# Kernel tuning notes

Measured on AMD Instinct MI355X. Metric: run time of the kernel, lower is better.

The kernel has to match this reference:

```python
import jax, jax.numpy as jnp
import numpy as np

B, T, C = 2, 2048, 1024
H, D, R = 16, 64, 32  # heads, head_dim, compression rank (R < D)


def setup_inputs() -> dict:
    key = jax.random.key(0)
    ks = jax.random.split(key, 8)
    s = 0.02
    return {
        "hidden_states": jax.random.normal(ks[0], (B, T, C), jnp.float32),
        "c_attn_w": jax.random.normal(ks[1], (C, 3 * C), jnp.float32) * s,
        "c_attn_b": jnp.zeros((3 * C,), jnp.float32),
        "c_proj_w": jax.random.normal(ks[2], (C, C), jnp.float32) * s,
        "c_proj_b": jnp.zeros((C,), jnp.float32),
        "wk_c": jax.random.normal(ks[3], (D, R), jnp.float32) * (1.0 / np.sqrt(D)),
        "wk_e": jax.random.normal(ks[4], (R, D), jnp.float32) * (1.0 / np.sqrt(R)),
        "wv_c": jax.random.normal(ks[5], (D, R), jnp.float32) * (1.0 / np.sqrt(D)),
        "wv_e": jax.random.normal(ks[6], (R, D), jnp.float32) * (1.0 / np.sqrt(R)),
    }


def reference(hidden_states, c_attn_w, c_attn_b, c_proj_w, c_proj_b,
              wk_c, wk_e, wv_c, wv_e):
    b, t, c = hidden_states.shape
    # GPT2 Conv1D: x @ W + b, then split into Q, K, V
    qkv = hidden_states @ c_attn_w + c_attn_b  # [B,T,3C]
    q, k, v = jnp.split(qkv, 3, axis=-1)

    def split_heads(x):  # [B,T,C] -> [B,H,T,D]
        return x.reshape(b, t, H, D).transpose(0, 2, 1, 3)

    q = split_heads(q)
    k = split_heads(k)
    v = split_heads(v)

    # Low-rank KV compression then expansion (rank R < D path)
    k_lat = jnp.einsum('bhtd,dr->bhtr', k, wk_c)  # [B,H,T,R]
    v_lat = jnp.einsum('bhtd,dr->bhtr', v, wv_c)
    k_exp = jnp.einsum('bhtr,rd->bhtd', k_lat, wk_e)  # [B,H,T,D]
    v_exp = jnp.einsum('bhtr,rd->bhtd', v_lat, wv_e)

    # Causal SDPA (attention_mask is None and q_len > 1 -> is_causal=True)
    scale = 1.0 / np.sqrt(D).astype(np.float32)
    scores = jnp.einsum('bhqd,bhkd->bhqk', q, k_exp) * scale  # [B,H,T,T]
    causal = jnp.tril(jnp.ones((t, t), dtype=bool))
    scores = jnp.where(causal[None, None], scores, jnp.finfo(scores.dtype).min)
    probs = jax.nn.softmax(scores, axis=-1)
    attn = jnp.einsum('bhqk,bhkd->bhqd', probs, v_exp)  # [B,H,T,D]

    # Merge heads and output projection
    attn = attn.transpose(0, 2, 1, 3).reshape(b, t, c)
    out = attn @ c_proj_w + c_proj_b
    return out
```

## Files before the change

kernel.cpp:

```cpp
#include <hip/hip_runtime.h>
#include <cstddef>

typedef __attribute__((ext_vector_type(8))) __bf16 bf16x8;
typedef __attribute__((ext_vector_type(4))) float f32x4;
typedef unsigned short u16;
typedef unsigned int   u32;

#define SCLF (0.125f * 1.44269504f)

__device__ __forceinline__ u16 f2bf(float f){
  union { float f; u32 u; } v; v.f = f;
  u32 r = v.u + 0x7FFFu + ((v.u >> 16) & 1u);
  return (u16)(r >> 16);
}
__device__ __forceinline__ u32 cvtpk(float lo, float hi){
  u32 r; asm("v_cvt_pk_bf16_f32 %0, %1, %2" : "=v"(r) : "v"(lo), "v"(hi)); return r;
}
__device__ __forceinline__ void gll16(const void* g, void* l){
  __builtin_amdgcn_global_load_lds((__attribute__((address_space(1))) void*)g,
                                   (__attribute__((address_space(3))) void*)l, 16, 0, 0);
}

__global__ __launch_bounds__(256) void convert_all(const float* __restrict__ x,
      const float* __restrict__ Wa, const float* __restrict__ ba,
      const float* __restrict__ kc, const float* __restrict__ ke,
      const float* __restrict__ vc, const float* __restrict__ ve,
      u16* __restrict__ Xb, u16* __restrict__ Wab, u16* __restrict__ Mb,
      float* __restrict__ b2){
  __shared__ float BaL[1024];
  __shared__ float W65[32*65];
  const int bid = blockIdx.x, tid = threadIdx.x;
  if (bid < 4096){
    int i = bid*256 + tid;
    float4 v = ((const float4*)x)[i];
    ushort4 r; r.x=f2bf(v.x); r.y=f2bf(v.y); r.z=f2bf(v.z); r.w=f2bf(v.w);
    ((ushort4*)Xb)[i] = r;
  } else if (bid < 7168){
    int i = (bid-4096)*256 + tid;
    float4 v = ((const float4*)Wa)[i];
    ushort4 r; r.x=f2bf(v.x); r.y=f2bf(v.y); r.z=f2bf(v.z); r.w=f2bf(v.w);
    ((ushort4*)Wab)[i] = r;
  } else if (bid == 7168){
    #pragma unroll
    for (int t=0;t<8;++t){
      int idx = t*256 + tid;
      Mb[idx] = f2bf(ke[idx]*SCLF);
      int d = idx>>5, r = idx&31;
      Mb[2048 + r*64 + d] = f2bf(kc[idx]);
      Mb[4096 + r*64 + d] = f2bf(vc[idx]);
      Mb[6144 + idx] = f2bf(ve[idx]);
    }
  } else {
    const int part = bid - 7169;
    *(float4*)&BaL[tid*4] = *(const float4*)&ba[part*1024 + tid*4];
    {
      const float* msrc = (part==0) ? ke : (part==1) ? kc : vc;
      #pragma unroll
      for (int i=0;i<8;++i){
        int idx = tid + i*256;
        float v = msrc[idx];
        int r, d;
        if (part == 0){ r = idx >> 6; d = idx & 63; }
        else          { d = idx >> 5; r = idx & 31; }
        W65[r*65 + d] = v;
      }
    }
    __syncthreads();
    const float scl = (part==0) ? SCLF : 1.f;
    #pragma unroll
    for (int t=0;t<2;++t){
      int l = tid + t*256;
      int hh = l >> 5, r = l & 31;
      float acc = 0.f;
      for (int d=0;d<64;++d) acc += BaL[hh*64 + d] * W65[r*65 + d];
      b2[part*512 + l] = acc * scl;
    }
  }
}

__global__ __launch_bounds__(256) void transpose_cvt(const float* __restrict__ src, int ld_src,
            u16* __restrict__ dst, int ld_dst){
  __shared__ float tile[64][65];
  int c0 = blockIdx.x*64, n0 = blockIdx.y*64;
  int tx = threadIdx.x & 63, ty = threadIdx.x >> 6;
  #pragma unroll 4
  for (int k=0;k<16;++k){
    int r = 4*k + ty;
    tile[r][tx] = src[(size_t)(c0+r)*ld_src + n0 + tx];
  }
  __syncthreads();
  #pragma unroll 4
  for (int k=0;k<16;++k){
    int r = 4*k + ty;
    dst[(size_t)(n0+r)*ld_dst + c0 + tx] = f2bf(tile[tx][r]);
  }
}

__global__ __launch_bounds__(256) void fold_gemm_qkv(const u16* __restrict__ Wab,
      const u16* __restrict__ Mb, u16* __restrict__ Wt){
  __shared__ u16 As[4096];
  __shared__ u16 Bs[2048];
  const int cc = blockIdx.x, ph = blockIdx.y;
  const int tid = threadIdx.x, wv = tid>>6, ln = tid&63;
  const int lr = ln&15, g8 = (ln>>4)*8, gq = ln>>4;
  const int c0 = cc*64;
  const u16* A = Wab + (size_t)c0*3072 + ph*64;
  const u16* B = Mb + (ph>>4)*2048;
  const int lrow = ln>>3, lcol = (ln&7)*8;
  #pragma unroll
  for (int it=0;it<3;++it){
    int c3 = wv*3 + it;
    if (c3 < 8) gll16(A + (size_t)(c3*8+lrow)*3072 + lcol, &As[c3*512]);
    else { int bc = c3-8; gll16(B + (bc*8+lrow)*64 + lcol, &Bs[bc*512]); }
  }
  __syncthreads();
  f32x4 acc[2] = {};
  const int wr = (wv>>1)*32, wn = wv&1;
  #pragma unroll
  for (int ks=0;ks<2;++ks){
    bf16x8 bf = *(const bf16x8*)&Bs[(wn*16+lr)*64 + ks*32 + g8];
    #pragma unroll
    for (int mt=0;mt<2;++mt){
      bf16x8 af = *(const bf16x8*)&As[(wr+mt*16+lr)*64 + ks*32 + g8];
      acc[mt] = __builtin_amdgcn_mfma_f32_16x16x32_bf16(af, bf, acc[mt], 0,0,0);
    }
  }
  const int n = (ph>>4)*512 + (ph&15)*32 + wn*16 + lr;
  #pragma unroll
  for (int mt=0;mt<2;++mt){
    union { u16 s[4]; uint2 v; } pk;
    #pragma unroll
    for (int r=0;r<4;++r) pk.s[r] = f2bf(acc[mt][r]);
    *(uint2*)&Wt[(size_t)n*1024 + c0 + wr + mt*16 + 4*gq] = pk.v;
  }
}

__global__ __launch_bounds__(256) void fold_gemm_proj(const u16* __restrict__ WpTb,
      const u16* __restrict__ veb, u16* __restrict__ W2t){
  __shared__ u16 As[4096];
  __shared__ u16 Bs[2048];
  const int cc = blockIdx.x, ph = blockIdx.y;
  const int tid = threadIdx.x, wv = tid>>6, ln = tid&63;
  const int lr = ln&15, g8 = (ln>>4)*8, gq = ln>>4;
  const int c0 = cc*64;
  const u16* A = WpTb + (size_t)c0*1024 + ph*64;
  const int lrow = ln>>3, lcol = (ln&7)*8;
  #pragma unroll
  for (int it=0;it<3;++it){
    int c3 = wv*3 + it;
    if (c3 < 8) gll16(A + (size_t)(c3*8+lrow)*1024 + lcol, &As[c3*512]);
    else { int bc = c3-8; gll16(veb + (bc*8+lrow)*64 + lcol, &Bs[bc*512]); }
  }
  __syncthreads();
  f32x4 acc[2] = {};
  const int wr = (wv>>1)*32, wn = wv&1;
  #pragma unroll
  for (int ks=0;ks<2;++ks){
    bf16x8 bf = *(const bf16x8*)&Bs[(wn*16+lr)*64 + ks*32 + g8];
    #pragma unroll
    for (int mt=0;mt<2;++mt){
      bf16x8 af = *(const bf16x8*)&As[(wr+mt*16+lr)*64 + ks*32 + g8];
      acc[mt] = __builtin_amdgcn_mfma_f32_16x16x32_bf16(af, bf, acc[mt], 0,0,0);
    }
  }
  const int col = ph*32 + wn*16 + lr;
  #pragma unroll
  for (int mt=0;mt<2;++mt)
    #pragma unroll
    for (int r=0;r<4;++r)
      W2t[(size_t)(c0 + wr + mt*16 + 4*gq + r)*512 + col] = f2bf(acc[mt][r]);
}

template<typename OT>
__global__ __launch_bounds__(256) void gemm64(const u16* __restrict__ A, const u16* __restrict__ Bt,
        const float* __restrict__ bias, OT* __restrict__ C, u16* __restrict__ Vt,
        int M, int N, int K, int ldc){
  __shared__ u16 As[64*64];
  __shared__ u16 Bs[128*64];
  const int nwg = gridDim.x * gridDim.y;
  const int id  = blockIdx.x + gridDim.x * blockIdx.y;
  const int nid = (id & 7) * (nwg >> 3) + (id >> 3);
  const int bx = nid % gridDim.x, by = nid / gridDim.x;
  const int tid = threadIdx.x, wv = tid>>6, ln = tid&63;
  const int lr = ln&15, g8 = (ln>>4)*8;
  const int m0 = bx*64, n0 = by*128;
  const int wr = (wv>>1)*32, wc = (wv&1)*64;
  const int lrow = ln>>3, lcol = (ln&7)*8;
  f32x4 acc[2][4] = {};
  const int nk = K >> 6;
  for (int kt=0; kt<nk; ++kt){
    #pragma unroll
    for (int it=0; it<6; ++it){
      int chunk = wv*6 + it;
      if (chunk < 8){
        int row = chunk*8 + lrow;
        gll16(A + (size_t)(m0+row)*K + kt*64 + lcol, &As[chunk*512]);
      } else {
        int bc = chunk - 8;
        int row = bc*8 + lrow;
        gll16(Bt + (size_t)(n0+row)*K + kt*64 + lcol, &Bs[bc*512]);
      }
    }
    __syncthreads();
    #pragma unroll
    for (int ks=0; ks<2; ++ks){
      bf16x8 af[2], bfr[4];
      #pragma unroll
      for (int mt=0;mt<2;++mt) af[mt]  = *(const bf16x8*)&As[(wr+mt*16+lr)*64 + ks*32 + g8];
      #pragma unroll
      for (int nt=0;nt<4;++nt) bfr[nt] = *(const bf16x8*)&Bs[(wc+nt*16+lr)*64 + ks*32 + g8];
      #pragma unroll
      for (int mt=0;mt<2;++mt)
        #pragma unroll
        for (int nt=0;nt<4;++nt)
          acc[mt][nt] = __builtin_amdgcn_mfma_f32_16x16x32_bf16(af[mt], bfr[nt], acc[mt][nt], 0,0,0);
    }
    __syncthreads();
  }
  if (Vt && n0 >= 1024){
    #pragma unroll
    for (int mt=0;mt<2;++mt){
      int row0 = m0 + wr + mt*16 + 4*(ln>>4);
      int tin  = row0 & 2047;
      int p0 = 4*((tin>>4)&1) + 8*((tin>>2)&3) + 32*(tin>>5);
      size_t vbase = (size_t)(row0 >> 11) * 512;
      #pragma unroll
      for (int nt=0;nt<4;++nt){
        int col = n0 + wc + nt*16 + lr;
        float bv = bias[col];
        int nlat = col - 1024;
        union { u16 s[4]; uint2 v; } pk;
        #pragma unroll
        for (int r=0;r<4;++r) pk.s[r] = f2bf(acc[mt][nt][r] + bv);
        *(uint2*)&Vt[(vbase + nlat)*2048 + p0] = pk.v;
      }
    }
  } else {
    #pragma unroll
    for (int mt=0;mt<2;++mt){
      int row = m0 + wr + mt*16 + 4*(ln>>4);
      #pragma unroll
      for (int nt=0;nt<4;++nt){
        int col = n0 + wc + nt*16 + lr;
        float bv = bias[col];
        #pragma unroll
        for (int r=0;r<4;++r){
          float v = acc[mt][nt][r] + bv;
          if constexpr (sizeof(OT) == 2) C[(size_t)(row+r)*ldc + col] = f2bf(v);
          else                           C[(size_t)(row+r)*ldc + col] = v;
        }
      }
    }
  }
}

__global__ __launch_bounds__(512, 8) void attn_fwd(const u16* __restrict__ QKV,
            const u16* __restrict__ Vt, u16* __restrict__ Out){
  const int bh = blockIdx.x;
  const int qt = 31 - blockIdx.y;
  const int b = bh >> 4, h = bh & 15;
  const int tid = threadIdx.x, wv = tid>>6, ln = tid&63;
  const int sg = wv>>2, wvL = wv&3;
  const int lr = ln&15, gq = ln>>4;
  __shared__ __align__(16) char SMEM[32768];
  u16* KB0 = (u16*)SMEM           + (sg*2    )*2048;
  u16* KB1 = (u16*)SMEM           + (sg*2 + 1)*2048;
  u16* VB0 = (u16*)(SMEM + 16384) + (sg*2    )*2048;
  u16* VB1 = (u16*)(SMEM + 16384) + (sg*2 + 1)*2048;
  const int q0 = qt*64;
  const size_t base = (size_t)(b*2048) * 1536;
  bf16x8 qf = *(const bf16x8*)(QKV + base + (size_t)(q0 + wvL*16 + lr)*1536 + h*32 + gq*8);
  const int qglob = q0 + wvL*16 + lr;
  f32x4 o0 = {}, o1 = {};
  float l_r = 0.f;
  const u16* ksrc = QKV + base + 512 + h*32;
  const u16* vsrc = Vt + (size_t)(bh*32)*2048;

  const int ci = wvL*64 + ln;
  const int rK = ci>>2, cK = 8*((ci&3) ^ (rK&3));
  const int rV = ci>>3, cV = 8*((ci&7) ^ (rV&7));

  int offK[4], offV[2][2];
  #pragma unroll
  for (int nt=0;nt<4;++nt)
    offK[nt] = (nt*16+lr)*64 + ((gq*16) ^ ((lr&3)<<4));
  #pragma unroll
  for (int dt=0;dt<2;++dt)
    #pragma unroll
    for (int c=0;c<2;++c)
      offV[dt][c] = (dt*16+lr)*128 + ((c*64 + gq*16) ^ ((lr&7)<<4));

  if (sg <= qt){
    gll16(ksrc + (size_t)(sg*64 + rK)*1536 + cK, KB0 + wvL*512);
    gll16(vsrc + (size_t)rV*2048 + sg*64 + cV,   VB0 + wvL*512);
  }
  __syncthreads();
  const u16* kp = ksrc + (size_t)(sg*64 + 128 + rK)*1536 + cK;
  const u16* vp = vsrc + (size_t)rV*2048 + sg*64 + 128 + cV;
  const size_t KSTEP = (size_t)128*1536;

  #define ABODY(II, KBC, VBC, KBN, VBN) do { \
    const int kt = 2*(II) + sg; \
    if (kt + 2 <= qt){ \
      gll16(kp, (KBN) + wvL*512); \
      gll16(vp, (VBN) + wvL*512); \
      kp += KSTEP; vp += 128; \
    } \
    if (kt <= qt){ \
      f32x4 s4[4] = {}; \
      __builtin_amdgcn_s_setprio(1); \
      _Pragma("unroll") for (int nt=0;nt<4;++nt){ \
        bf16x8 k0 = *(const bf16x8*)((const char*)(KBC) + offK[nt]); \
        s4[nt] = __builtin_amdgcn_mfma_f32_16x16x32_bf16(k0, qf, s4[nt], 0,0,0); \
      } \
      __builtin_amdgcn_s_setprio(0); \
      if (kt == qt){ \
        const int kv0 = kt*64; \
        _Pragma("unroll") for (int nt=0;nt<4;++nt) \
        _Pragma("unroll") for (int r=0;r<4;++r){ \
          int k = kv0 + nt*16 + 4*gq + r; \
          if (k > qglob) s4[nt][r] = -1e30f; \
        } \
      } \
      float p0,p1,p2,p3,p4,p5,p6,p7; \
      p0=__builtin_amdgcn_exp2f(s4[0][0]); p1=__builtin_amdgcn_exp2f(s4[0][1]); \
      p2=__builtin_amdgcn_exp2f(s4[0][2]); p3=__builtin_amdgcn_exp2f(s4[0][3]); \
      p4=__builtin_amdgcn_exp2f(s4[1][0]); p5=__builtin_amdgcn_exp2f(s4[1][1]); \
      p6=__builtin_amdgcn_exp2f(s4[1][2]); p7=__builtin_amdgcn_exp2f(s4[1][3]); \
      l_r += ((p0+p1)+(p2+p3)) + ((p4+p5)+(p6+p7)); \
      union { u32 u[4]; bf16x8 v; } pa0, pa1; \
      pa0.u[0]=cvtpk(p0,p1); pa0.u[1]=cvtpk(p2,p3); pa0.u[2]=cvtpk(p4,p5); pa0.u[3]=cvtpk(p6,p7); \
      p0=__builtin_amdgcn_exp2f(s4[2][0]); p1=__builtin_amdgcn_exp2f(s4[2][1]); \
      p2=__builtin_amdgcn_exp2f(s4[2][2]); p3=__builtin_amdgcn_exp2f(s4[2][3]); \
      p4=__builtin_amdgcn_exp2f(s4[3][0]); p5=__builtin_amdgcn_exp2f(s4[3][1]); \
      p6=__builtin_amdgcn_exp2f(s4[3][2]); p7=__builtin_amdgcn_exp2f(s4[3][3]); \
      l_r += ((p0+p1)+(p2+p3)) + ((p4+p5)+(p6+p7)); \
      pa1.u[0]=cvtpk(p0,p1); pa1.u[1]=cvtpk(p2,p3); pa1.u[2]=cvtpk(p4,p5); pa1.u[3]=cvtpk(p6,p7); \
      __builtin_amdgcn_s_setprio(1); \
      o0 = __builtin_amdgcn_mfma_f32_16x16x32_bf16(pa0.v, *(const bf16x8*)((const char*)(VBC) + offV[0][0]), o0, 0,0,0); \
      o1 = __builtin_amdgcn_mfma_f32_16x16x32_bf16(pa0.v, *(const bf16x8*)((const char*)(VBC) + offV[1][0]), o1, 0,0,0); \
      o0 = __builtin_amdgcn_mfma_f32_16x16x32_bf16(pa1.v, *(const bf16x8*)((const char*)(VBC) + offV[0][1]), o0, 0,0,0); \
      o1 = __builtin_amdgcn_mfma_f32_16x16x32_bf16(pa1.v, *(const bf16x8*)((const char*)(VBC) + offV[1][1]), o1, 0,0,0); \
      __builtin_amdgcn_s_setprio(0); \
    } \
    __syncthreads(); \
  } while(0)

  const int nmax = (qt + 2) >> 1;
  const int jmax = (nmax + 1) >> 1;
  for (int j = 0; j < jmax; ++j){
    ABODY(2*j,   KB0, VB0, KB1, VB1);
    ABODY(2*j+1, KB1, VB1, KB0, VB0);
  }
  l_r += __shfl_xor(l_r, 16);
  l_r += __shfl_xor(l_r, 32);

  float* MO = (float*)SMEM;
  float* ML = (float*)(SMEM + 12288);
  if (sg == 1){
    #pragma unroll
    for (int r=0;r<4;++r){
      MO[(wvL*16 + 4*gq + r)*34 + lr]      = o0[r];
      MO[(wvL*16 + 4*gq + r)*34 + 16 + lr] = o1[r];
    }
    if (gq == 0) ML[wvL*16 + lr] = l_r;
  }
  __syncthreads();
  if (sg == 0){
    float lS = l_r + ML[wvL*16 + lr];
    float lS_o[4];
    #pragma unroll
    for (int r=0;r<4;++r) lS_o[r] = __shfl(lS, 4*gq + r);
    #pragma unroll
    for (int r=0;r<4;++r){
      int orow = wvL*16 + 4*gq + r;
      float v0 = (o0[r] + MO[orow*34 + lr])      / lS_o[r];
      float v1 = (o1[r] + MO[orow*34 + 16 + lr]) / lS_o[r];
      size_t ob = (size_t)(b*2048 + q0 + orow)*512 + h*32;
      Out[ob + lr]      = f2bf(v0);
      Out[ob + 16 + lr] = f2bf(v1);
    }
  }
}

#define WS_B2   0u
#define WS_WT   8192u
#define WS_W2T  (WS_WT + 3145728u)
#define WS_XB   (WS_W2T + 1048576u)
#define WS_QKV  (WS_XB + 8388608u)
#define WS_VT   (WS_QKV + 12582912u)
#define WS_ATT  (WS_VT + 4194304u)
#define WS_WAB  (WS_ATT + 4194304u)
#define WS_WPT  (WS_WAB + 6291456u)
#define WS_MB   (WS_WPT + 2097152u)

extern "C" void kernel_launch(void* const* d_in, const int* in_sizes, int n_in,
                              void* d_out, int out_size, void* d_ws, size_t ws_size,
                              hipStream_t stream) {
  const float* x  = (const float*)d_in[0];
  const float* Wa = (const float*)d_in[1];
  const float* ba = (const float*)d_in[2];
  const float* Wp = (const float*)d_in[3];
  const float* bp = (const float*)d_in[4];
  const float* kc = (const float*)d_in[5];
  const float* ke = (const float*)d_in[6];
  const float* vc = (const float*)d_in[7];
  const float* ve = (const float*)d_in[8];
  float* out = (float*)d_out;
  char* ws = (char*)d_ws;
  float* b2  = (float*)(ws + WS_B2);
  u16* Wt    = (u16*)(ws + WS_WT);
  u16* W2t   = (u16*)(ws + WS_W2T);
  u16* Xb    = (u16*)(ws + WS_XB);
  u16* QKVb  = (u16*)(ws + WS_QKV);
  u16* Vt    = (u16*)(ws + WS_VT);
  u16* Att   = (u16*)(ws + WS_ATT);
  u16* Wab   = (u16*)(ws + WS_WAB);
  u16* WpTb  = (u16*)(ws + WS_WPT);
  u16* Mb    = (u16*)(ws + WS_MB);
  u16* veb   = Mb + 6144;

  convert_all<<<7172, 256, 0, stream>>>(x, Wa, ba, kc, ke, vc, ve, Xb, Wab, Mb, b2);
  transpose_cvt<<<dim3(16,16), 256, 0, stream>>>(Wp, 1024, WpTb, 1024);
  fold_gemm_qkv<<<dim3(16,48), 256, 0, stream>>>(Wab, Mb, Wt);
  fold_gemm_proj<<<dim3(16,16), 256, 0, stream>>>(WpTb, veb, W2t);
  gemm64<u16><<<dim3(64,12), 256, 0, stream>>>(Xb, Wt, b2, QKVb, Vt, 4096, 1536, 1024, 1536);
  attn_fwd<<<dim3(32,32), 512, 0, stream>>>(QKVb, Vt, Att);
  gemm64<float><<<dim3(64,8), 256, 0, stream>>>(Att, W2t, bp, out, (u16*)nullptr, 4096, 1024, 512, 1024);
}
```

Baseline: 84.13 us.

## Merge prep kernels and give attention waves two query subtiles each

The Wp transpose-convert is folded into convert_all, and the two fold GEMMs are merged into one launch. Together these cut the weight-prep stage from four launches to two and remove launch gaps. The attention kernel moves from 8 to 4 waves per block. Each wave now processes two 16-row query subtiles that share the same K and V fragment loads, which improves LDS reuse and MFMA density. The cost is higher register pressure and fewer waves per block for hiding latency.

```diff
diff --git a/kernel.cpp b/kernel.cpp
--- a/kernel.cpp
+++ b/kernel.cpp
@@ -22,13 +22,12 @@
 }
 
 __global__ __launch_bounds__(256) void convert_all(const float* __restrict__ x,
-      const float* __restrict__ Wa, const float* __restrict__ ba,
+      const float* __restrict__ Wa, const float* __restrict__ ba, const float* __restrict__ Wp,
       const float* __restrict__ kc, const float* __restrict__ ke,
       const float* __restrict__ vc, const float* __restrict__ ve,
       u16* __restrict__ Xb, u16* __restrict__ Wab, u16* __restrict__ Mb,
-      float* __restrict__ b2){
-  __shared__ float BaL[1024];
-  __shared__ float W65[32*65];
+      float* __restrict__ b2, u16* __restrict__ WpTb){
+  __shared__ float SH[4160];
   const int bid = blockIdx.x, tid = threadIdx.x;
   if (bid < 4096){
     int i = bid*256 + tid;
@@ -50,8 +49,10 @@
       Mb[4096 + r*64 + d] = f2bf(vc[idx]);
       Mb[6144 + idx] = f2bf(ve[idx]);
     }
-  } else {
+  } else if (bid < 7172){
     const int part = bid - 7169;
+    float* BaL = SH;
+    float* W65 = SH + 1024;
     *(float4*)&BaL[tid*4] = *(const float4*)&ba[part*1024 + tid*4];
     {
       const float* msrc = (part==0) ? ke : (part==1) ? kc : vc;
@@ -75,42 +76,44 @@
       for (int d=0;d<64;++d) acc += BaL[hh*64 + d] * W65[r*65 + d];
       b2[part*512 + l] = acc * scl;
     }
-  }
-}
-
-__global__ __launch_bounds__(256) void transpose_cvt(const float* __restrict__ src, int ld_src,
-            u16* __restrict__ dst, int ld_dst){
-  __shared__ float tile[64][65];
-  int c0 = blockIdx.x*64, n0 = blockIdx.y*64;
-  int tx = threadIdx.x & 63, ty = threadIdx.x >> 6;
-  #pragma unroll 4
-  for (int k=0;k<16;++k){
-    int r = 4*k + ty;
-    tile[r][tx] = src[(size_t)(c0+r)*ld_src + n0 + tx];
-  }
-  __syncthreads();
-  #pragma unroll 4
-  for (int k=0;k<16;++k){
-    int r = 4*k + ty;
-    dst[(size_t)(n0+r)*ld_dst + c0 + tx] = f2bf(tile[tx][r]);
-  }
-}
-
-__global__ __launch_bounds__(256) void fold_gemm_qkv(const u16* __restrict__ Wab,
-      const u16* __restrict__ Mb, u16* __restrict__ Wt){
+  } else {
+    const int idx2 = bid - 7172;
+    const int c0 = (idx2 & 15)*64, n0 = (idx2 >> 4)*64;
+    float* tile = SH;
+    int tx = tid & 63, ty = tid >> 6;
+    #pragma unroll 4
+    for (int k=0;k<16;++k){
+      int r = 4*k + ty;
+      tile[r*65 + tx] = Wp[(size_t)(c0+r)*1024 + n0 + tx];
+    }
+    __syncthreads();
+    #pragma unroll 4
+    for (int k=0;k<16;++k){
+      int r = 4*k + ty;
+      WpTb[(size_t)(n0+r)*1024 + c0 + tx] = f2bf(tile[tx*65 + r]);
+    }
+  }
+}
+
+__global__ __launch_bounds__(256) void fold_gemms(const u16* __restrict__ Wab,
+      const u16* __restrict__ Mb, const u16* __restrict__ WpTb,
+      u16* __restrict__ Wt, u16* __restrict__ W2t){
   __shared__ u16 As[4096];
   __shared__ u16 Bs[2048];
-  const int cc = blockIdx.x, ph = blockIdx.y;
+  const int cc = blockIdx.x, y = blockIdx.y;
   const int tid = threadIdx.x, wv = tid>>6, ln = tid&63;
   const int lr = ln&15, g8 = (ln>>4)*8, gq = ln>>4;
   const int c0 = cc*64;
-  const u16* A = Wab + (size_t)c0*3072 + ph*64;
-  const u16* B = Mb + (ph>>4)*2048;
   const int lrow = ln>>3, lcol = (ln&7)*8;
+  const bool qkv = (y < 48);
+  const int ph = qkv ? y : (y - 48);
+  const u16* A = qkv ? (Wab + (size_t)c0*3072 + ph*64) : (WpTb + (size_t)c0*1024 + ph*64);
+  const u16* B = qkv ? (Mb + (ph>>4)*2048) : (Mb + 6144);
+  const size_t astr = qkv ? 3072 : 1024;
   #pragma unroll
   for (int it=0;it<3;++it){
     int c3 = wv*3 + it;
-    if (c3 < 8) gll16(A + (size_t)(c3*8+lrow)*3072 + lcol, &As[c3*512]);
+    if (c3 < 8) gll16(A + (size_t)(c3*8+lrow)*astr + lcol, &As[c3*512]);
     else { int bc = c3-8; gll16(B + (bc*8+lrow)*64 + lcol, &Bs[bc*512]); }
   }
   __syncthreads();
@@ -125,50 +128,23 @@
       acc[mt] = __builtin_amdgcn_mfma_f32_16x16x32_bf16(af, bf, acc[mt], 0,0,0);
     }
   }
-  const int n = (ph>>4)*512 + (ph&15)*32 + wn*16 + lr;
-  #pragma unroll
-  for (int mt=0;mt<2;++mt){
-    union { u16 s[4]; uint2 v; } pk;
-    #pragma unroll
-    for (int r=0;r<4;++r) pk.s[r] = f2bf(acc[mt][r]);
-    *(uint2*)&Wt[(size_t)n*1024 + c0 + wr + mt*16 + 4*gq] = pk.v;
-  }
-}
-
-__global__ __launch_bounds__(256) void fold_gemm_proj(const u16* __restrict__ WpTb,
-      const u16* __restrict__ veb, u16* __restrict__ W2t){
-  __shared__ u16 As[4096];
-  __shared__ u16 Bs[2048];
-  const int cc = blockIdx.x, ph = blockIdx.y;
-  const int tid = threadIdx.x, wv = tid>>6, ln = tid&63;
-  const int lr = ln&15, g8 = (ln>>4)*8, gq = ln>>4;
-  const int c0 = cc*64;
-  const u16* A = WpTb + (size_t)c0*1024 + ph*64;
-  const int lrow = ln>>3, lcol = (ln&7)*8;
-  #pragma unroll
-  for (int it=0;it<3;++it){
-    int c3 = wv*3 + it;
-    if (c3 < 8) gll16(A + (size_t)(c3*8+lrow)*1024 + lcol, &As[c3*512]);
-    else { int bc = c3-8; gll16(veb + (bc*8+lrow)*64 + lcol, &Bs[bc*512]); }
-  }
-  __syncthreads();
-  f32x4 acc[2] = {};
-  const int wr = (wv>>1)*32, wn = wv&1;
-  #pragma unroll
-  for (int ks=0;ks<2;++ks){
-    bf16x8 bf = *(const bf16x8*)&Bs[(wn*16+lr)*64 + ks*32 + g8];
+  if (qkv){
+    const int n = (ph>>4)*512 + (ph&15)*32 + wn*16 + lr;
     #pragma unroll
     for (int mt=0;mt<2;++mt){
-      bf16x8 af = *(const bf16x8*)&As[(wr+mt*16+lr)*64 + ks*32 + g8];
-      acc[mt] = __builtin_amdgcn_mfma_f32_16x16x32_bf16(af, bf, acc[mt], 0,0,0);
-    }
-  }
-  const int col = ph*32 + wn*16 + lr;
-  #pragma unroll
-  for (int mt=0;mt<2;++mt)
-    #pragma unroll
-    for (int r=0;r<4;++r)
-      W2t[(size_t)(c0 + wr + mt*16 + 4*gq + r)*512 + col] = f2bf(acc[mt][r]);
+      union { u16 s[4]; uint2 v; } pk;
+      #pragma unroll
+      for (int r=0;r<4;++r) pk.s[r] = f2bf(acc[mt][r]);
+      *(uint2*)&Wt[(size_t)n*1024 + c0 + wr + mt*16 + 4*gq] = pk.v;
+    }
+  } else {
+    const int col = ph*32 + wn*16 + lr;
+    #pragma unroll
+    for (int mt=0;mt<2;++mt)
+      #pragma unroll
+      for (int r=0;r<4;++r)
+        W2t[(size_t)(c0 + wr + mt*16 + 4*gq + r)*512 + col] = f2bf(acc[mt][r]);
+  }
 }
 
 template<typename OT>
@@ -254,13 +230,13 @@
   }
 }
 
-__global__ __launch_bounds__(512, 8) void attn_fwd(const u16* __restrict__ QKV,
+__global__ __launch_bounds__(256, 4) void attn_fwd(const u16* __restrict__ QKV,
             const u16* __restrict__ Vt, u16* __restrict__ Out){
   const int bh = blockIdx.x;
   const int qt = 31 - blockIdx.y;
   const int b = bh >> 4, h = bh & 15;
   const int tid = threadIdx.x, wv = tid>>6, ln = tid&63;
-  const int sg = wv>>2, wvL = wv&3;
+  const int sg = wv>>1, wvL = wv&1;
   const int lr = ln&15, gq = ln>>4;
   __shared__ __align__(16) char SMEM[32768];
   u16* KB0 = (u16*)SMEM           + (sg*2    )*2048;
@@ -269,10 +245,12 @@
   u16* VB1 = (u16*)(SMEM + 16384) + (sg*2 + 1)*2048;
   const int q0 = qt*64;
   const size_t base = (size_t)(b*2048) * 1536;
-  bf16x8 qf = *(const bf16x8*)(QKV + base + (size_t)(q0 + wvL*16 + lr)*1536 + h*32 + gq*8);
-  const int qglob = q0 + wvL*16 + lr;
-  f32x4 o0 = {}, o1 = {};
-  float l_r = 0.f;
+  const u16* qrowA = QKV + base + (size_t)(q0 + wvL*32 + lr)*1536 + h*32;
+  bf16x8 qfA = *(const bf16x8*)(qrowA + gq*8);
+  bf16x8 qfB = *(const bf16x8*)(qrowA + (size_t)16*1536 + gq*8);
+  const int qgA = q0 + wvL*32 + lr, qgB = qgA + 16;
+  f32x4 oA0 = {}, oA1 = {}, oB0 = {}, oB1 = {};
+  float lA = 0.f, lB = 0.f;
   const u16* ksrc = QKV + base + 512 + h*32;
   const u16* vsrc = Vt + (size_t)(bh*32)*2048;
 
@@ -291,27 +269,34 @@
       offV[dt][c] = (dt*16+lr)*128 + ((c*64 + gq*16) ^ ((lr&7)<<4));
 
   if (sg <= qt){
-    gll16(ksrc + (size_t)(sg*64 + rK)*1536 + cK, KB0 + wvL*512);
-    gll16(vsrc + (size_t)rV*2048 + sg*64 + cV,   VB0 + wvL*512);
+    gll16(ksrc + (size_t)(sg*64 + rK)*1536 + cK,      KB0 + wvL*512);
+    gll16(ksrc + (size_t)(sg*64 + 32 + rK)*1536 + cK, KB0 + 1024 + wvL*512);
+    gll16(vsrc + (size_t)rV*2048 + sg*64 + cV,        VB0 + wvL*512);
+    gll16(vsrc + (size_t)(16+rV)*2048 + sg*64 + cV,   VB0 + 1024 + wvL*512);
   }
   __syncthreads();
-  const u16* kp = ksrc + (size_t)(sg*64 + 128 + rK)*1536 + cK;
-  const u16* vp = vsrc + (size_t)rV*2048 + sg*64 + 128 + cV;
+  const u16* kpa = ksrc + (size_t)(sg*64 + 128 + rK)*1536 + cK;
+  const u16* kpb = ksrc + (size_t)(sg*64 + 160 + rK)*1536 + cK;
+  const u16* vpa = vsrc + (size_t)rV*2048 + sg*64 + 128 + cV;
+  const u16* vpb = vsrc + (size_t)(16+rV)*2048 + sg*64 + 128 + cV;
   const size_t KSTEP = (size_t)128*1536;
 
   #define ABODY(II, KBC, VBC, KBN, VBN) do { \
     const int kt = 2*(II) + sg; \
     if (kt + 2 <= qt){ \
-      gll16(kp, (KBN) + wvL*512); \
-      gll16(vp, (VBN) + wvL*512); \
-      kp += KSTEP; vp += 128; \
+      gll16(kpa, (KBN) + wvL*512); \
+      gll16(kpb, (KBN) + 1024 + wvL*512); \
+      gll16(vpa, (VBN) + wvL*512); \
+      gll16(vpb, (VBN) + 1024 + wvL*512); \
+      kpa += KSTEP; kpb += KSTEP; vpa += 128; vpb += 128; \
     } \
     if (kt <= qt){ \
-      f32x4 s4[4] = {}; \
+      f32x4 sA[4] = {}, sB[4] = {}; \
       __builtin_amdgcn_s_setprio(1); \
       _Pragma("unroll") for (int nt=0;nt<4;++nt){ \
         bf16x8 k0 = *(const bf16x8*)((const char*)(KBC) + offK[nt]); \
-        s4[nt] = __builtin_amdgcn_mfma_f32_16x16x32_bf16(k0, qf, s4[nt], 0,0,0); \
+        sA[nt] = __builtin_amdgcn_mfma_f32_16x16x32_bf16(k0, qfA, sA[nt], 0,0,0); \
+        sB[nt] = __builtin_amdgcn_mfma_f32_16x16x32_bf16(k0, qfB, sB[nt], 0,0,0); \
       } \
       __builtin_amdgcn_s_setprio(0); \
       if (kt == qt){ \
@@ -319,28 +304,53 @@
         _Pragma("unroll") for (int nt=0;nt<4;++nt) \
         _Pragma("unroll") for (int r=0;r<4;++r){ \
           int k = kv0 + nt*16 + 4*gq + r; \
-          if (k > qglob) s4[nt][r] = -1e30f; \
+          if (k > qgA) sA[nt][r] = -1e30f; \
+          if (k > qgB) sB[nt][r] = -1e30f; \
         } \
       } \
-      float p0,p1,p2,p3,p4,p5,p6,p7; \
-      p0=__builtin_amdgcn_exp2f(s4[0][0]); p1=__builtin_amdgcn_exp2f(s4[0][1]); \
-      p2=__builtin_amdgcn_exp2f(s4[0][2]); p3=__builtin_amdgcn_exp2f(s4[0][3]); \
-      p4=__builtin_amdgcn_exp2f(s4[1][0]); p5=__builtin_amdgcn_exp2f(s4[1][1]); \
-      p6=__builtin_amdgcn_exp2f(s4[1][2]); p7=__builtin_amdgcn_exp2f(s4[1][3]); \
-      l_r += ((p0+p1)+(p2+p3)) + ((p4+p5)+(p6+p7)); \
-      union { u32 u[4]; bf16x8 v; } pa0, pa1; \
-      pa0.u[0]=cvtpk(p0,p1); pa0.u[1]=cvtpk(p2,p3); pa0.u[2]=cvtpk(p4,p5); pa0.u[3]=cvtpk(p6,p7); \
-      p0=__builtin_amdgcn_exp2f(s4[2][0]); p1=__builtin_amdgcn_exp2f(s4[2][1]); \
-      p2=__builtin_amdgcn_exp2f(s4[2][2]); p3=__builtin_amdgcn_exp2f(s4[2][3]); \
-      p4=__builtin_amdgcn_exp2f(s4[3][0]); p5=__builtin_amdgcn_exp2f(s4[3][1]); \
-      p6=__builtin_amdgcn_exp2f(s4[3][2]); p7=__builtin_amdgcn_exp2f(s4[3][3]); \
-      l_r += ((p0+p1)+(p2+p3)) + ((p4+p5)+(p6+p7)); \
-      pa1.u[0]=cvtpk(p0,p1); pa1.u[1]=cvtpk(p2,p3); pa1.u[2]=cvtpk(p4,p5); pa1.u[3]=cvtpk(p6,p7); \
+      union { u32 u[4]; bf16x8 v; } paA0, paA1, paB0, paB1; \
+      { \
+        float p0,p1,p2,p3,p4,p5,p6,p7; \
+        p0=__builtin_amdgcn_exp2f(sA[0][0]); p1=__builtin_amdgcn_exp2f(sA[0][1]); \
+        p2=__builtin_amdgcn_exp2f(sA[0][2]); p3=__builtin_amdgcn_exp2f(sA[0][3]); \
+        p4=__builtin_amdgcn_exp2f(sA[1][0]); p5=__builtin_amdgcn_exp2f(sA[1][1]); \
+        p6=__builtin_amdgcn_exp2f(sA[1][2]); p7=__builtin_amdgcn_exp2f(sA[1][3]); \
+        lA += ((p0+p1)+(p2+p3)) + ((p4+p5)+(p6+p7)); \
+        paA0.u[0]=cvtpk(p0,p1); paA0.u[1]=cvtpk(p2,p3); paA0.u[2]=cvtpk(p4,p5); paA0.u[3]=cvtpk(p6,p7); \
+        p0=__builtin_amdgcn_exp2f(sA[2][0]); p1=__builtin_amdgcn_exp2f(sA[2][1]); \
+        p2=__builtin_amdgcn_exp2f(sA[2][2]); p3=__builtin_amdgcn_exp2f(sA[2][3]); \
+        p4=__builtin_amdgcn_exp2f(sA[3][0]); p5=__builtin_amdgcn_exp2f(sA[3][1]); \
+        p6=__builtin_amdgcn_exp2f(sA[3][2]); p7=__builtin_amdgcn_exp2f(sA[3][3]); \
+        lA += ((p0+p1)+(p2+p3)) + ((p4+p5)+(p6+p7)); \
+        paA1.u[0]=cvtpk(p0,p1); paA1.u[1]=cvtpk(p2,p3); paA1.u[2]=cvtpk(p4,p5); paA1.u[3]=cvtpk(p6,p7); \
+        p0=__builtin_amdgcn_exp2f(sB[0][0]); p1=__builtin_amdgcn_exp2f(sB[0][1]); \
+        p2=__builtin_amdgcn_exp2f(sB[0][2]); p3=__builtin_amdgcn_exp2f(sB[0][3]); \
+        p4=__builtin_amdgcn_exp2f(sB[1][0]); p5=__builtin_amdgcn_exp2f(sB[1][1]); \
+        p6=__builtin_amdgcn_exp2f(sB[1][2]); p7=__builtin_amdgcn_exp2f(sB[1][3]); \
+        lB += ((p0+p1)+(p2+p3)) + ((p4+p5)+(p6+p7)); \
+        paB0.u[0]=cvtpk(p0,p1); paB0.u[1]=cvtpk(p2,p3); paB0.u[2]=cvtpk(p4,p5); paB0.u[3]=cvtpk(p6,p7); \
+        p0=__builtin_amdgcn_exp2f(sB[2][0]); p1=__builtin_amdgcn_exp2f(sB[2][1]); \
+        p2=__builtin_amdgcn_exp2f(sB[2][2]); p3=__builtin_amdgcn_exp2f(sB[2][3]); \
+        p4=__builtin_amdgcn_exp2f(sB[3][0]); p5=__builtin_amdgcn_exp2f(sB[3][1]); \
+        p6=__builtin_amdgcn_exp2f(sB[3][2]); p7=__builtin_amdgcn_exp2f(sB[3][3]); \
+        lB += ((p0+p1)+(p2+p3)) + ((p4+p5)+(p6+p7)); \
+        paB1.u[0]=cvtpk(p0,p1); paB1.u[1]=cvtpk(p2,p3); paB1.u[2]=cvtpk(p4,p5); paB1.u[3]=cvtpk(p6,p7); \
+      } \
       __builtin_amdgcn_s_setprio(1); \
-      o0 = __builtin_amdgcn_mfma_f32_16x16x32_bf16(pa0.v, *(const bf16x8*)((const char*)(VBC) + offV[0][0]), o0, 0,0,0); \
-      o1 = __builtin_amdgcn_mfma_f32_16x16x32_bf16(pa0.v, *(const bf16x8*)((const char*)(VBC) + offV[1][0]), o1, 0,0,0); \
-      o0 = __builtin_amdgcn_mfma_f32_16x16x32_bf16(pa1.v, *(const bf16x8*)((const char*)(VBC) + offV[0][1]), o0, 0,0,0); \
-      o1 = __builtin_amdgcn_mfma_f32_16x16x32_bf16(pa1.v, *(const bf16x8*)((const char*)(VBC) + offV[1][1]), o1, 0,0,0); \
+      { \
+        bf16x8 v00 = *(const bf16x8*)((const char*)(VBC) + offV[0][0]); \
+        bf16x8 v10 = *(const bf16x8*)((const char*)(VBC) + offV[1][0]); \
+        bf16x8 v01 = *(const bf16x8*)((const char*)(VBC) + offV[0][1]); \
+        bf16x8 v11 = *(const bf16x8*)((const char*)(VBC) + offV[1][1]); \
+        oA0 = __builtin_amdgcn_mfma_f32_16x16x32_bf16(paA0.v, v00, oA0, 0,0,0); \
+        oA1 = __builtin_amdgcn_mfma_f32_16x16x32_bf16(paA0.v, v10, oA1, 0,0,0); \
+        oB0 = __builtin_amdgcn_mfma_f32_16x16x32_bf16(paB0.v, v00, oB0, 0,0,0); \
+        oB1 = __builtin_amdgcn_mfma_f32_16x16x32_bf16(paB0.v, v10, oB1, 0,0,0); \
+        oA0 = __builtin_amdgcn_mfma_f32_16x16x32_bf16(paA1.v, v01, oA0, 0,0,0); \
+        oA1 = __builtin_amdgcn_mfma_f32_16x16x32_bf16(paA1.v, v11, oA1, 0,0,0); \
+        oB0 = __builtin_amdgcn_mfma_f32_16x16x32_bf16(paB1.v, v01, oB0, 0,0,0); \
+        oB1 = __builtin_amdgcn_mfma_f32_16x16x32_bf16(paB1.v, v11, oB1, 0,0,0); \
+      } \
       __builtin_amdgcn_s_setprio(0); \
     } \
     __syncthreads(); \
@@ -352,33 +362,42 @@
     ABODY(2*j,   KB0, VB0, KB1, VB1);
     ABODY(2*j+1, KB1, VB1, KB0, VB0);
   }
-  l_r += __shfl_xor(l_r, 16);
-  l_r += __shfl_xor(l_r, 32);
+  lA += __shfl_xor(lA, 16); lA += __shfl_xor(lA, 32);
+  lB += __shfl_xor(lB, 16); lB += __shfl_xor(lB, 32);
 
   float* MO = (float*)SMEM;
   float* ML = (float*)(SMEM + 12288);
   if (sg == 1){
     #pragma unroll
     for (int r=0;r<4;++r){
-      MO[(wvL*16 + 4*gq + r)*34 + lr]      = o0[r];
-      MO[(wvL*16 + 4*gq + r)*34 + 16 + lr] = o1[r];
-    }
-    if (gq == 0) ML[wvL*16 + lr] = l_r;
+      int rowA = wvL*32 + 4*gq + r;
+      MO[rowA*34 + lr]            = oA0[r];
+      MO[rowA*34 + 16 + lr]       = oA1[r];
+      MO[(rowA+16)*34 + lr]       = oB0[r];
+      MO[(rowA+16)*34 + 16 + lr]  = oB1[r];
+    }
+    if (gq == 0){ ML[wvL*32 + lr] = lA; ML[wvL*32 + 16 + lr] = lB; }
   }
   __syncthreads();
   if (sg == 0){
-    float lS = l_r + ML[wvL*16 + lr];
-    float lS_o[4];
-    #pragma unroll
-    for (int r=0;r<4;++r) lS_o[r] = __shfl(lS, 4*gq + r);
+    float lSA = lA + ML[wvL*32 + lr];
+    float lSB = lB + ML[wvL*32 + 16 + lr];
+    float lA_o[4], lB_o[4];
+    #pragma unroll
+    for (int r=0;r<4;++r){ lA_o[r] = __shfl(lSA, 4*gq + r); lB_o[r] = __shfl(lSB, 4*gq + r); }
     #pragma unroll
     for (int r=0;r<4;++r){
-      int orow = wvL*16 + 4*gq + r;
-      float v0 = (o0[r] + MO[orow*34 + lr])      / lS_o[r];
-      float v1 = (o1[r] + MO[orow*34 + 16 + lr]) / lS_o[r];
-      size_t ob = (size_t)(b*2048 + q0 + orow)*512 + h*32;
-      Out[ob + lr]      = f2bf(v0);
-      Out[ob + 16 + lr] = f2bf(v1);
+      int rowA = wvL*32 + 4*gq + r;
+      float vA0 = (oA0[r] + MO[rowA*34 + lr])           / lA_o[r];
+      float vA1 = (oA1[r] + MO[rowA*34 + 16 + lr])      / lA_o[r];
+      float vB0 = (oB0[r] + MO[(rowA+16)*34 + lr])      / lB_o[r];
+      float vB1 = (oB1[r] + MO[(rowA+16)*34 + 16 + lr]) / lB_o[r];
+      size_t obA = (size_t)(b*2048 + q0 + rowA)*512 + h*32;
+      Out[obA + lr]      = f2bf(vA0);
+      Out[obA + 16 + lr] = f2bf(vA1);
+      size_t obB = obA + (size_t)16*512;
+      Out[obB + lr]      = f2bf(vB0);
+      Out[obB + 16 + lr] = f2bf(vB1);
     }
   }
 }
@@ -418,13 +437,10 @@
   u16* Wab   = (u16*)(ws + WS_WAB);
   u16* WpTb  = (u16*)(ws + WS_WPT);
   u16* Mb    = (u16*)(ws + WS_MB);
-  u16* veb   = Mb + 6144;
-
-  convert_all<<<7172, 256, 0, stream>>>(x, Wa, ba, kc, ke, vc, ve, Xb, Wab, Mb, b2);
-  transpose_cvt<<<dim3(16,16), 256, 0, stream>>>(Wp, 1024, WpTb, 1024);
-  fold_gemm_qkv<<<dim3(16,48), 256, 0, stream>>>(Wab, Mb, Wt);
-  fold_gemm_proj<<<dim3(16,16), 256, 0, stream>>>(WpTb, veb, W2t);
+
+  convert_all<<<7428, 256, 0, stream>>>(x, Wa, ba, Wp, kc, ke, vc, ve, Xb, Wab, Mb, b2, WpTb);
+  fold_gemms<<<dim3(16,64), 256, 0, stream>>>(Wab, Mb, WpTb, Wt, W2t);
   gemm64<u16><<<dim3(64,12), 256, 0, stream>>>(Xb, Wt, b2, QKVb, Vt, 4096, 1536, 1024, 1536);
-  attn_fwd<<<dim3(32,32), 512, 0, stream>>>(QKVb, Vt, Att);
+  attn_fwd<<<dim3(32,32), 256, 0, stream>>>(QKVb, Vt, Att);
   gemm64<float><<<dim3(64,8), 256, 0, stream>>>(Att, W2t, bp, out, (u16*)nullptr, 4096, 1024, 512, 1024);
 }
```

Measured after the change: 80.08 us. -4.8%, faster.
